# Kernel optimization log

Hardware: AMD Instinct MI355X
Metric: run time of the kernel (lower is better)

Reference implementation:

```python
import jax, jax.numpy as jnp
import numpy as np

M, N, D = 8192, 8192, 64

def setup_inputs() -> dict:
    key = jax.random.key(0)
    k1, k2 = jax.random.split(key)
    X = jax.random.normal(k1, (M, D), dtype=jnp.float32)
    Y = jax.random.normal(k2, (N, D), dtype=jnp.float32)
    gamma_param = jnp.asarray(1.0, dtype=jnp.float32)  # learnable scalar (rbf branch)
    return {"X": X, "Y": Y, "gamma_param": gamma_param}

def reference(X, Y, gamma_param):
    # RBF kernel: exp(-gamma * ||x_i - y_j||^2), (m, n)
    x_sq = jnp.sum(X * X, axis=-1)          # (m,)
    y_sq = jnp.sum(Y * Y, axis=-1)          # (n,)
    xy = jnp.einsum("md,nd->mn", X, Y)      # (m, n)
    sq_norm = x_sq[:, None] + y_sq[None, :] - 2.0 * xy
    sq_norm = jnp.maximum(sq_norm, 0.0)     # numerical clamp
    return jnp.exp(-gamma_param * sq_norm)
```

## Files before the change

kernel.cpp:

```cpp
#include <hip/hip_runtime.h>

#define MTOT 8192
#define NTOT 8192
#define DD   64
#define SPLIT (MTOT * DD)

typedef __bf16 bf16x8 __attribute__((ext_vector_type(8)));
typedef float  f32x16 __attribute__((ext_vector_type(16)));
typedef unsigned short u16;
typedef unsigned short u16x4 __attribute__((ext_vector_type(4)));
typedef unsigned short u16x8 __attribute__((ext_vector_type(8)));

__device__ __forceinline__ u16 bf16_rne(float v) {
    unsigned int u = __float_as_uint(v);
    u = u + 0x7FFFu + ((u >> 16) & 1u);
    return (u16)(u >> 16);
}
__device__ __forceinline__ float bf16_to_f32(u16 h) {
    return __uint_as_float(((unsigned int)h) << 16);
}

#define MFMA(a, b, c) __builtin_amdgcn_mfma_f32_32x32x16_bf16((a), (b), (c), 0, 0, 0)

__global__ __launch_bounds__(256)
void rbf_pre_kernel(const float* __restrict__ X, const float* __restrict__ Y,
                    u16* __restrict__ XhiF, u16* __restrict__ XloF,
                    u16* __restrict__ YhiF, u16* __restrict__ YloF,
                    float* __restrict__ xqs, float* __restrict__ yqs)
{
    const int gid = blockIdx.x * 256 + threadIdx.x;
    const int mat = gid >> 15;
    const int r4  = gid & 32767;
    const int row = r4 >> 2;
    const int q   = r4 & 3;
    const float* src = mat ? Y : X;
    u16* hi  = mat ? YhiF : XhiF;
    u16* lo  = mat ? YloF : XloF;
    float* nrm = mat ? yqs : xqs;

    const long rbase = (long)row * DD + q * 16;
    float s = 0.f;
    u16x8 h0, h1, l0, l1;
    #pragma unroll
    for (int c = 0; c < 4; ++c) {
        const float4 v = *reinterpret_cast<const float4*>(src + rbase + c * 4);
        const float vv[4] = {v.x, v.y, v.z, v.w};
        #pragma unroll
        for (int e = 0; e < 4; ++e) {
            const int idx = c * 4 + e;
            const float x = vv[e];
            s = fmaf(x, x, s);
            const u16 hh = bf16_rne(x);
            const u16 ll = bf16_rne(x - bf16_to_f32(hh));
            if (idx < 8) { h0[idx] = hh; l0[idx] = ll; }
            else         { h1[idx - 8] = hh; l1[idx - 8] = ll; }
        }
    }
    s += __shfl_xor(s, 1);
    s += __shfl_xor(s, 2);
    if (q == 0) nrm[row] = s;

    const int tt = row >> 5, lr = row & 31;
    const long fbase = (long)(tt * 4 + q) * 512;
    *reinterpret_cast<u16x8*>(hi + fbase + lr * 8)        = h0;
    *reinterpret_cast<u16x8*>(hi + fbase + (32 + lr) * 8) = h1;
    *reinterpret_cast<u16x8*>(lo + fbase + lr * 8)        = l0;
    *reinterpret_cast<u16x8*>(lo + fbase + (32 + lr) * 8) = l1;
}

__global__ __launch_bounds__(256, 2)
void rbf_main_kernel(const u16* __restrict__ XhiF, const u16* __restrict__ XloF,
                     const u16* __restrict__ YhiF, const u16* __restrict__ YloF,
                     const float* __restrict__ xqs, const float* __restrict__ yqs,
                     const float* __restrict__ gamma_p,
                     float* __restrict__ out)
{
    __shared__ __align__(16) u16 S[4][8192];

    const int t = threadIdx.x;
    const int w = t >> 6;
    const int l = t & 63;

    const int bid = blockIdx.x;
    const int swz = ((bid & 7) << 9) | (bid >> 3);
    const int bm = swz >> 6;
    const int bn = swz & 63;
    const long row0 = (long)bm * 128;
    const long col0 = (long)bn * 128;

    const u16* gsrc;
    if      (w == 0) gsrc = XhiF + (long)bm * 8192;
    else if (w == 1) gsrc = XloF + (long)bm * 8192;
    else if (w == 2) gsrc = YhiF + (long)bn * 8192;
    else             gsrc = YloF + (long)bn * 8192;
    u16* const ldst = &S[w][0];
    #pragma unroll
    for (int c = 0; c < 16; ++c) {
        const int off = c * 512 + l * 8;
        *reinterpret_cast<int4*>(ldst + off) = *reinterpret_cast<const int4*>(gsrc + off);
    }
    __syncthreads();

    const int mt0 = (w >> 1) * 2;
    const int nt0 = (w & 1) * 2;

    bf16x8 aH[2][4], aL[2][4];
    #pragma unroll
    for (int i = 0; i < 2; ++i)
        #pragma unroll
        for (int ks = 0; ks < 4; ++ks) {
            aH[i][ks] = *reinterpret_cast<const bf16x8*>(&S[0][((mt0 + i) * 4 + ks) * 512 + l * 8]);
            aL[i][ks] = *reinterpret_cast<const bf16x8*>(&S[1][((mt0 + i) * 4 + ks) * 512 + l * 8]);
        }

    f32x16 acc[2][2];
    #pragma unroll
    for (int i = 0; i < 2; ++i)
        #pragma unroll
        for (int j = 0; j < 2; ++j)
            #pragma unroll
            for (int r = 0; r < 16; ++r) acc[i][j][r] = 0.f;

    #pragma unroll
    for (int ks = 0; ks < 4; ++ks) {
        const bf16x8 b0h = *reinterpret_cast<const bf16x8*>(&S[2][((nt0 + 0) * 4 + ks) * 512 + l * 8]);
        const bf16x8 b1h = *reinterpret_cast<const bf16x8*>(&S[2][((nt0 + 1) * 4 + ks) * 512 + l * 8]);
        const bf16x8 b0l = *reinterpret_cast<const bf16x8*>(&S[3][((nt0 + 0) * 4 + ks) * 512 + l * 8]);
        const bf16x8 b1l = *reinterpret_cast<const bf16x8*>(&S[3][((nt0 + 1) * 4 + ks) * 512 + l * 8]);
        acc[0][0] = MFMA(aH[0][ks], b0h, acc[0][0]);
        acc[0][1] = MFMA(aH[0][ks], b1h, acc[0][1]);
        acc[1][0] = MFMA(aH[1][ks], b0h, acc[1][0]);
        acc[1][1] = MFMA(aH[1][ks], b1h, acc[1][1]);
        acc[0][0] = MFMA(aH[0][ks], b0l, acc[0][0]);
        acc[0][1] = MFMA(aH[0][ks], b1l, acc[0][1]);
        acc[1][0] = MFMA(aH[1][ks], b0l, acc[1][0]);
        acc[1][1] = MFMA(aH[1][ks], b1l, acc[1][1]);
        acc[0][0] = MFMA(aL[0][ks], b0h, acc[0][0]);
        acc[0][1] = MFMA(aL[0][ks], b1h, acc[0][1]);
        acc[1][0] = MFMA(aL[1][ks], b0h, acc[1][0]);
        acc[1][1] = MFMA(aL[1][ks], b1h, acc[1][1]);
    }

    const float g  = gamma_p[0];
    const float g2 = 2.0f * g;
    const int l5x4 = (l >> 5) * 4;
    const int ln   = l & 31;

    #pragma unroll
    for (int i = 0; i < 2; ++i) {
        const int mt = mt0 + i;
        float xv[16];
        #pragma unroll
        for (int p = 0; p < 4; ++p) {
            const float4 x4 = *reinterpret_cast<const float4*>(xqs + row0 + mt * 32 + 8 * p + l5x4);
            xv[p * 4 + 0] = x4.x; xv[p * 4 + 1] = x4.y;
            xv[p * 4 + 2] = x4.z; xv[p * 4 + 3] = x4.w;
        }
        #pragma unroll
        for (int j = 0; j < 2; ++j) {
            const int nt = nt0 + j;
            const long gc = col0 + nt * 32 + ln;
            const float cy = -g * yqs[gc];
            float* const obase = out + gc;
            #pragma unroll
            for (int r = 0; r < 16; ++r) {
                float arg = fmaf(g2, acc[i][j][r], fmaf(-g, xv[r], cy));
                arg = fminf(arg, 0.f);
                const long rr = row0 + mt * 32 + (r & 3) + 8 * (r >> 2) + l5x4;
                __builtin_nontemporal_store(__expf(arg), obase + rr * (long)NTOT);
            }
        }
    }
}

__global__ __launch_bounds__(256, 2)
void rbf_fallback_kernel(const float* __restrict__ X,
                         const float* __restrict__ Y,
                         const float* __restrict__ gamma_p,
                         float* __restrict__ out)
{
    __shared__ unsigned short XfH[4][4][64][8];
    __shared__ unsigned short XfL[4][4][64][8];
    __shared__ unsigned short YfH[4][4][64][8];
    __shared__ unsigned short YfL[4][4][64][8];
    __shared__ float xq[128];
    __shared__ float yq[128];

    const int t = threadIdx.x;
    const long row0 = (long)blockIdx.y * 128;
    const long col0 = (long)blockIdx.x * 128;

    {
        const int k0   = (t & 15) * 4;
        const int ks   = k0 >> 4;
        const int l32  = ((k0 >> 3) & 1) << 5;
        const int slot = k0 & 4;
        #pragma unroll
        for (int i = 0; i < 8; ++i) {
            const int row  = (t >> 4) + i * 16;
            const int mt   = row >> 5;
            const int lane = (row & 31) | l32;
            const float4 vx = *reinterpret_cast<const float4*>(X + (row0 + row) * DD + k0);
            const float4 vy = *reinterpret_cast<const float4*>(Y + (col0 + row) * DD + k0);
            float xv[4] = {vx.x, vx.y, vx.z, vx.w};
            float yv[4] = {vy.x, vy.y, vy.z, vy.w};
            u16x4 xh, xl, yh, yl;
            #pragma unroll
            for (int e = 0; e < 4; ++e) {
                const u16 hx = bf16_rne(xv[e]);
                xh[e] = hx; xl[e] = bf16_rne(xv[e] - bf16_to_f32(hx));
                const u16 hy = bf16_rne(yv[e]);
                yh[e] = hy; yl[e] = bf16_rne(yv[e] - bf16_to_f32(hy));
            }
            *reinterpret_cast<u16x4*>(&XfH[mt][ks][lane][slot]) = xh;
            *reinterpret_cast<u16x4*>(&XfL[mt][ks][lane][slot]) = xl;
            *reinterpret_cast<u16x4*>(&YfH[mt][ks][lane][slot]) = yh;
            *reinterpret_cast<u16x4*>(&YfL[mt][ks][lane][slot]) = yl;
        }
    }
    {
        const int r = t & 127;
        const float* p = (t < 128) ? (X + (row0 + r) * DD) : (Y + (col0 + r) * DD);
        float s0 = 0.f, s1 = 0.f, s2 = 0.f, s3 = 0.f;
        #pragma unroll
        for (int c = 0; c < 16; ++c) {
            const float4 v = reinterpret_cast<const float4*>(p)[c];
            s0 = fmaf(v.x, v.x, s0); s1 = fmaf(v.y, v.y, s1);
            s2 = fmaf(v.z, v.z, s2); s3 = fmaf(v.w, v.w, s3);
        }
        const float s = (s0 + s1) + (s2 + s3);
        if (t < 128) xq[r] = s; else yq[r] = s;
    }
    __syncthreads();

    const int w = t >> 6;
    const int l = t & 63;
    const int mt0 = (w >> 1) * 2;
    const int nt0 = (w & 1) * 2;

    bf16x8 aH[2][4], aL[2][4];
    #pragma unroll
    for (int i = 0; i < 2; ++i)
        #pragma unroll
        for (int ks = 0; ks < 4; ++ks) {
            aH[i][ks] = *reinterpret_cast<const bf16x8*>(&XfH[mt0 + i][ks][l][0]);
            aL[i][ks] = *reinterpret_cast<const bf16x8*>(&XfL[mt0 + i][ks][l][0]);
        }

    f32x16 acc[2][2];
    #pragma unroll
    for (int i = 0; i < 2; ++i)
        #pragma unroll
        for (int j = 0; j < 2; ++j)
            #pragma unroll
            for (int r = 0; r < 16; ++r) acc[i][j][r] = 0.f;

    #pragma unroll
    for (int ks = 0; ks < 4; ++ks) {
        const bf16x8 b0h = *reinterpret_cast<const bf16x8*>(&YfH[nt0 + 0][ks][l][0]);
        const bf16x8 b1h = *reinterpret_cast<const bf16x8*>(&YfH[nt0 + 1][ks][l][0]);
        const bf16x8 b0l = *reinterpret_cast<const bf16x8*>(&YfL[nt0 + 0][ks][l][0]);
        const bf16x8 b1l = *reinterpret_cast<const bf16x8*>(&YfL[nt0 + 1][ks][l][0]);
        acc[0][0] = MFMA(aH[0][ks], b0h, acc[0][0]);
        acc[0][1] = MFMA(aH[0][ks], b1h, acc[0][1]);
        acc[1][0] = MFMA(aH[1][ks], b0h, acc[1][0]);
        acc[1][1] = MFMA(aH[1][ks], b1h, acc[1][1]);
        acc[0][0] = MFMA(aH[0][ks], b0l, acc[0][0]);
        acc[0][1] = MFMA(aH[0][ks], b1l, acc[0][1]);
        acc[1][0] = MFMA(aH[1][ks], b0l, acc[1][0]);
        acc[1][1] = MFMA(aH[1][ks], b1l, acc[1][1]);
        acc[0][0] = MFMA(aL[0][ks], b0h, acc[0][0]);
        acc[0][1] = MFMA(aL[0][ks], b1h, acc[0][1]);
        acc[1][0] = MFMA(aL[1][ks], b0h, acc[1][0]);
        acc[1][1] = MFMA(aL[1][ks], b1h, acc[1][1]);
    }

    const float g = gamma_p[0];
    const int l5x4 = (l >> 5) * 4;
    const int ln = l & 31;
    #pragma unroll
    for (int i = 0; i < 2; ++i) {
        const int mt = mt0 + i;
        float xv[16];
        #pragma unroll
        for (int r = 0; r < 16; ++r)
            xv[r] = xq[mt * 32 + (r & 3) + 8 * (r >> 2) + l5x4];
        #pragma unroll
        for (int j = 0; j < 2; ++j) {
            const int nt = nt0 + j;
            const float yv = yq[nt * 32 + ln];
            const long gr = row0 + mt * 32;
            const long gc = col0 + nt * 32 + ln;
            #pragma unroll
            for (int r = 0; r < 16; ++r) {
                float s = fmaf(-2.f, acc[i][j][r], xv[r] + yv);
                s = fmaxf(s, 0.f);
                const long rr = gr + (r & 3) + 8 * (r >> 2) + l5x4;
                out[rr * NTOT + gc] = __expf(-g * s);
            }
        }
    }
}

extern "C" void kernel_launch(void* const* d_in, const int* in_sizes, int n_in,
                              void* d_out, int out_size, void* d_ws, size_t ws_size,
                              hipStream_t stream) {
    (void)in_sizes; (void)n_in; (void)out_size;
    const float* X = (const float*)d_in[0];
    const float* Y = (const float*)d_in[1];
    const float* gamma_p = (const float*)d_in[2];
    float* out = (float*)d_out;

    const size_t need = 4 * (size_t)SPLIT * sizeof(u16) + (MTOT + NTOT) * sizeof(float);

    if (ws_size >= need) {
        u16* XhiF = (u16*)d_ws;
        u16* XloF = XhiF + SPLIT;
        u16* YhiF = XloF + SPLIT;
        u16* YloF = YhiF + SPLIT;
        float* xqs = (float*)(YloF + SPLIT);
        float* yqs = xqs + MTOT;
        rbf_pre_kernel<<<256, 256, 0, stream>>>(X, Y, XhiF, XloF, YhiF, YloF, xqs, yqs);
        rbf_main_kernel<<<4096, 256, 0, stream>>>(XhiF, XloF, YhiF, YloF, xqs, yqs, gamma_p, out);
    } else {
        dim3 grid(NTOT / 128, MTOT / 128);
        rbf_fallback_kernel<<<grid, 256, 0, stream>>>(X, Y, gamma_p, out);
    }
}
```

Measured before the change: 56.13 us.

## Make RBF main kernel persistent, reusing X tiles and prefetching Y via LDS DMA

Replaces the one-tile-per-block main kernel with a 512-block persistent kernel. Each block keeps its X hi/lo tile resident and iterates over 8 column tiles. Y tiles are loaded with global_load_lds DMA, and the next one is issued before the exp/store epilogue so the load overlaps output writes. This removes repeated X loads and per-block launch and setup cost, but adds per-iteration barriers and less block-level parallelism for hiding store latency.

```diff
diff --git a/kernel.cpp b/kernel.cpp
--- a/kernel.cpp
+++ b/kernel.cpp
@@ -21,6 +21,13 @@
 }
 
 #define MFMA(a, b, c) __builtin_amdgcn_mfma_f32_32x32x16_bf16((a), (b), (c), 0, 0, 0)
+
+__device__ __forceinline__ void load_lds_16B(const u16* g, u16* lds_uniform) {
+    __builtin_amdgcn_global_load_lds(
+        (const __attribute__((address_space(1))) unsigned int*)g,
+        (__attribute__((address_space(3))) unsigned int*)lds_uniform,
+        16, 0, 0);
+}
 
 __global__ __launch_bounds__(256)
 void rbf_pre_kernel(const float* __restrict__ X, const float* __restrict__ Y,
@@ -69,107 +76,135 @@
 }
 
 __global__ __launch_bounds__(256, 2)
-void rbf_main_kernel(const u16* __restrict__ XhiF, const u16* __restrict__ XloF,
-                     const u16* __restrict__ YhiF, const u16* __restrict__ YloF,
-                     const float* __restrict__ xqs, const float* __restrict__ yqs,
-                     const float* __restrict__ gamma_p,
-                     float* __restrict__ out)
+void rbf_persist_kernel(const u16* __restrict__ XhiF, const u16* __restrict__ XloF,
+                        const u16* __restrict__ YhiF, const u16* __restrict__ YloF,
+                        const float* __restrict__ xqs, const float* __restrict__ yqs,
+                        const float* __restrict__ gamma_p,
+                        float* __restrict__ out)
 {
-    __shared__ __align__(16) u16 S[4][8192];
+    __shared__ __align__(16) u16 Xbuf[16384];
+    __shared__ __align__(16) u16 Ybuf[16384];
 
     const int t = threadIdx.x;
     const int w = t >> 6;
     const int l = t & 63;
 
-    const int bid = blockIdx.x;
-    const int swz = ((bid & 7) << 9) | (bid >> 3);
-    const int bm = swz >> 6;
-    const int bn = swz & 63;
+    const int p   = blockIdx.x;
+    const int xcd = p & 7;
+    const int i   = p >> 3;
+    const int bm  = xcd * 8 + (i >> 3);
+    const int bn0 = i & 7;
     const long row0 = (long)bm * 128;
-    const long col0 = (long)bn * 128;
-
-    const u16* gsrc;
-    if      (w == 0) gsrc = XhiF + (long)bm * 8192;
-    else if (w == 1) gsrc = XloF + (long)bm * 8192;
-    else if (w == 2) gsrc = YhiF + (long)bn * 8192;
-    else             gsrc = YloF + (long)bn * 8192;
-    u16* const ldst = &S[w][0];
-    #pragma unroll
-    for (int c = 0; c < 16; ++c) {
-        const int off = c * 512 + l * 8;
-        *reinterpret_cast<int4*>(ldst + off) = *reinterpret_cast<const int4*>(gsrc + off);
-    }
-    __syncthreads();
-
-    const int mt0 = (w >> 1) * 2;
-    const int nt0 = (w & 1) * 2;
-
-    bf16x8 aH[2][4], aL[2][4];
-    #pragma unroll
-    for (int i = 0; i < 2; ++i)
-        #pragma unroll
-        for (int ks = 0; ks < 4; ++ks) {
-            aH[i][ks] = *reinterpret_cast<const bf16x8*>(&S[0][((mt0 + i) * 4 + ks) * 512 + l * 8]);
-            aL[i][ks] = *reinterpret_cast<const bf16x8*>(&S[1][((mt0 + i) * 4 + ks) * 512 + l * 8]);
-        }
-
-    f32x16 acc[2][2];
-    #pragma unroll
-    for (int i = 0; i < 2; ++i)
-        #pragma unroll
-        for (int j = 0; j < 2; ++j)
-            #pragma unroll
-            for (int r = 0; r < 16; ++r) acc[i][j][r] = 0.f;
-
-    #pragma unroll
-    for (int ks = 0; ks < 4; ++ks) {
-        const bf16x8 b0h = *reinterpret_cast<const bf16x8*>(&S[2][((nt0 + 0) * 4 + ks) * 512 + l * 8]);
-        const bf16x8 b1h = *reinterpret_cast<const bf16x8*>(&S[2][((nt0 + 1) * 4 + ks) * 512 + l * 8]);
-        const bf16x8 b0l = *reinterpret_cast<const bf16x8*>(&S[3][((nt0 + 0) * 4 + ks) * 512 + l * 8]);
-        const bf16x8 b1l = *reinterpret_cast<const bf16x8*>(&S[3][((nt0 + 1) * 4 + ks) * 512 + l * 8]);
-        acc[0][0] = MFMA(aH[0][ks], b0h, acc[0][0]);
-        acc[0][1] = MFMA(aH[0][ks], b1h, acc[0][1]);
-        acc[1][0] = MFMA(aH[1][ks], b0h, acc[1][0]);
-        acc[1][1] = MFMA(aH[1][ks], b1h, acc[1][1]);
-        acc[0][0] = MFMA(aH[0][ks], b0l, acc[0][0]);
-        acc[0][1] = MFMA(aH[0][ks], b1l, acc[0][1]);
-        acc[1][0] = MFMA(aH[1][ks], b0l, acc[1][0]);
-        acc[1][1] = MFMA(aH[1][ks], b1l, acc[1][1]);
-        acc[0][0] = MFMA(aL[0][ks], b0h, acc[0][0]);
-        acc[0][1] = MFMA(aL[0][ks], b1h, acc[0][1]);
-        acc[1][0] = MFMA(aL[1][ks], b0h, acc[1][0]);
-        acc[1][1] = MFMA(aL[1][ks], b1h, acc[1][1]);
+
+    {
+        const u16* xh = XhiF + (long)bm * 8192;
+        const u16* xl = XloF + (long)bm * 8192;
+        const u16* yh = YhiF + (long)bn0 * 8192;
+        const u16* yl = YloF + (long)bn0 * 8192;
+        #pragma unroll
+        for (int cc = 0; cc < 8; ++cc) {
+            const int c = w * 8 + cc;
+            const u16* gx = (c < 16) ? (xh + c * 512) : (xl + (c - 16) * 512);
+            const u16* gy = (c < 16) ? (yh + c * 512) : (yl + (c - 16) * 512);
+            load_lds_16B(gx + l * 8, &Xbuf[c * 512]);
+            load_lds_16B(gy + l * 8, &Ybuf[c * 512]);
+        }
     }
 
     const float g  = gamma_p[0];
     const float g2 = 2.0f * g;
+    const int  mt0 = (w >> 1) * 2;
+    const int  nt0 = (w & 1) * 2;
     const int l5x4 = (l >> 5) * 4;
-    const int ln   = l & 31;
-
-    #pragma unroll
-    for (int i = 0; i < 2; ++i) {
-        const int mt = mt0 + i;
-        float xv[16];
-        #pragma unroll
-        for (int p = 0; p < 4; ++p) {
-            const float4 x4 = *reinterpret_cast<const float4*>(xqs + row0 + mt * 32 + 8 * p + l5x4);
-            xv[p * 4 + 0] = x4.x; xv[p * 4 + 1] = x4.y;
-            xv[p * 4 + 2] = x4.z; xv[p * 4 + 3] = x4.w;
-        }
-        #pragma unroll
-        for (int j = 0; j < 2; ++j) {
-            const int nt = nt0 + j;
-            const long gc = col0 + nt * 32 + ln;
-            const float cy = -g * yqs[gc];
-            float* const obase = out + gc;
-            #pragma unroll
-            for (int r = 0; r < 16; ++r) {
-                float arg = fmaf(g2, acc[i][j][r], fmaf(-g, xv[r], cy));
-                arg = fminf(arg, 0.f);
-                const long rr = row0 + mt * 32 + (r & 3) + 8 * (r >> 2) + l5x4;
-                __builtin_nontemporal_store(__expf(arg), obase + rr * (long)NTOT);
+    const int  ln  = l & 31;
+
+    float xv[2][16];
+    #pragma unroll
+    for (int ii = 0; ii < 2; ++ii)
+        #pragma unroll
+        for (int q4 = 0; q4 < 4; ++q4) {
+            const float4 x4 = *reinterpret_cast<const float4*>(
+                xqs + row0 + (mt0 + ii) * 32 + 8 * q4 + l5x4);
+            xv[ii][q4 * 4 + 0] = x4.x; xv[ii][q4 * 4 + 1] = x4.y;
+            xv[ii][q4 * 4 + 2] = x4.z; xv[ii][q4 * 4 + 3] = x4.w;
+        }
+
+    __syncthreads();
+
+    bf16x8 aH[2][4], aL[2][4];
+    #pragma unroll
+    for (int ii = 0; ii < 2; ++ii)
+        #pragma unroll
+        for (int ks = 0; ks < 4; ++ks) {
+            aH[ii][ks] = *reinterpret_cast<const bf16x8*>(&Xbuf[((mt0 + ii) * 4 + ks) * 512 + l * 8]);
+            aL[ii][ks] = *reinterpret_cast<const bf16x8*>(&Xbuf[8192 + ((mt0 + ii) * 4 + ks) * 512 + l * 8]);
+        }
+
+    for (int it = 0; it < 8; ++it) {
+        const int  bn   = bn0 + 8 * it;
+        const long col0 = (long)bn * 128;
+
+        f32x16 acc[2][2];
+        #pragma unroll
+        for (int ii = 0; ii < 2; ++ii)
+            #pragma unroll
+            for (int jj = 0; jj < 2; ++jj)
+                #pragma unroll
+                for (int r = 0; r < 16; ++r) acc[ii][jj][r] = 0.f;
+
+        #pragma unroll
+        for (int ks = 0; ks < 4; ++ks) {
+            const bf16x8 b0h = *reinterpret_cast<const bf16x8*>(&Ybuf[((nt0 + 0) * 4 + ks) * 512 + l * 8]);
+            const bf16x8 b1h = *reinterpret_cast<const bf16x8*>(&Ybuf[((nt0 + 1) * 4 + ks) * 512 + l * 8]);
+            const bf16x8 b0l = *reinterpret_cast<const bf16x8*>(&Ybuf[8192 + ((nt0 + 0) * 4 + ks) * 512 + l * 8]);
+            const bf16x8 b1l = *reinterpret_cast<const bf16x8*>(&Ybuf[8192 + ((nt0 + 1) * 4 + ks) * 512 + l * 8]);
+            acc[0][0] = MFMA(aH[0][ks], b0h, acc[0][0]);
+            acc[0][1] = MFMA(aH[0][ks], b1h, acc[0][1]);
+            acc[1][0] = MFMA(aH[1][ks], b0h, acc[1][0]);
+            acc[1][1] = MFMA(aH[1][ks], b1h, acc[1][1]);
+            acc[0][0] = MFMA(aH[0][ks], b0l, acc[0][0]);
+            acc[0][1] = MFMA(aH[0][ks], b1l, acc[0][1]);
+            acc[1][0] = MFMA(aH[1][ks], b0l, acc[1][0]);
+            acc[1][1] = MFMA(aH[1][ks], b1l, acc[1][1]);
+            acc[0][0] = MFMA(aL[0][ks], b0h, acc[0][0]);
+            acc[0][1] = MFMA(aL[0][ks], b1h, acc[0][1]);
+            acc[1][0] = MFMA(aL[1][ks], b0h, acc[1][0]);
+            acc[1][1] = MFMA(aL[1][ks], b1h, acc[1][1]);
+        }
+
+        __syncthreads();
+
+        if (it < 7) {
+            const int bnn = bn0 + 8 * (it + 1);
+            const u16* yh = YhiF + (long)bnn * 8192;
+            const u16* yl = YloF + (long)bnn * 8192;
+            #pragma unroll
+            for (int cc = 0; cc < 8; ++cc) {
+                const int c = w * 8 + cc;
+                const u16* gy = (c < 16) ? (yh + c * 512) : (yl + (c - 16) * 512);
+                load_lds_16B(gy + l * 8, &Ybuf[c * 512]);
             }
         }
+
+        #pragma unroll
+        for (int ii = 0; ii < 2; ++ii) {
+            const int mt = mt0 + ii;
+            float* const orow = out + (row0 + mt * 32) * (long)NTOT;
+            #pragma unroll
+            for (int jj = 0; jj < 2; ++jj) {
+                const long gc = col0 + (nt0 + jj) * 32 + ln;
+                const float cy = -g * yqs[gc];
+                #pragma unroll
+                for (int r = 0; r < 16; ++r) {
+                    float arg = fmaf(g2, acc[ii][jj][r], fmaf(-g, xv[ii][r], cy));
+                    arg = fminf(arg, 0.f);
+                    const int rr = (r & 3) + 8 * (r >> 2) + l5x4;
+                    __builtin_nontemporal_store(__expf(arg), orow + rr * (long)NTOT + gc);
+                }
+            }
+        }
+
+        if (it < 7) __syncthreads();
     }
 }
 
@@ -220,11 +255,11 @@
     }
     {
         const int r = t & 127;
-        const float* p = (t < 128) ? (X + (row0 + r) * DD) : (Y + (col0 + r) * DD);
+        const float* p2 = (t < 128) ? (X + (row0 + r) * DD) : (Y + (col0 + r) * DD);
         float s0 = 0.f, s1 = 0.f, s2 = 0.f, s3 = 0.f;
         #pragma unroll
         for (int c = 0; c < 16; ++c) {
-            const float4 v = reinterpret_cast<const float4*>(p)[c];
+            const float4 v = reinterpret_cast<const float4*>(p2)[c];
             s0 = fmaf(v.x, v.x, s0); s1 = fmaf(v.y, v.y, s1);
             s2 = fmaf(v.z, v.z, s2); s3 = fmaf(v.w, v.w, s3);
         }
@@ -321,7 +356,7 @@
         float* xqs = (float*)(YloF + SPLIT);
         float* yqs = xqs + MTOT;
         rbf_pre_kernel<<<256, 256, 0, stream>>>(X, Y, XhiF, XloF, YhiF, YloF, xqs, yqs);
-        rbf_main_kernel<<<4096, 256, 0, stream>>>(XhiF, XloF, YhiF, YloF, xqs, yqs, gamma_p, out);
+        rbf_persist_kernel<<<512, 256, 0, stream>>>(XhiF, XloF, YhiF, YloF, xqs, yqs, gamma_p, out);
     } else {
         dim3 grid(NTOT / 128, MTOT / 128);
         rbf_fallback_kernel<<<grid, 256, 0, stream>>>(X, Y, gamma_p, out);
```

Result: slower. 61.84 us (+10.2%).

## Load MFMA fragments directly from global memory, dropping LDS staging

Applied to the files above, without the earlier changes.

The main kernel no longer stages the pre-swizzled bf16 hi/lo fragments through 64 KB of shared memory. Each wave now reads its A and B fragments straight from global memory, with a one-step register prefetch across the k-loop, and the occupancy hint rises from 2 to 3 blocks per CU. This removes the LDS round trip and the block barrier, and the freed shared memory can allow more resident blocks to hide the store-bound epilogue. In exchange, each fragment is read twice from global/L2 (once by each of two waves) instead of once per block.

```diff
diff --git a/kernel.cpp b/kernel.cpp
--- a/kernel.cpp
+++ b/kernel.cpp
@@ -68,18 +68,17 @@
     *reinterpret_cast<u16x8*>(lo + fbase + (32 + lr) * 8) = l1;
 }
 
-__global__ __launch_bounds__(256, 2)
-void rbf_main_kernel(const u16* __restrict__ XhiF, const u16* __restrict__ XloF,
-                     const u16* __restrict__ YhiF, const u16* __restrict__ YloF,
-                     const float* __restrict__ xqs, const float* __restrict__ yqs,
-                     const float* __restrict__ gamma_p,
-                     float* __restrict__ out)
+__global__ __launch_bounds__(256, 3)
+void rbf_nolds_kernel(const u16* __restrict__ XhiF, const u16* __restrict__ XloF,
+                      const u16* __restrict__ YhiF, const u16* __restrict__ YloF,
+                      const float* __restrict__ xqs, const float* __restrict__ yqs,
+                      const float* __restrict__ gamma_p,
+                      float* __restrict__ out)
 {
-    __shared__ __align__(16) u16 S[4][8192];
-
     const int t = threadIdx.x;
     const int w = t >> 6;
     const int l = t & 63;
+    const int loff = l * 8;
 
     const int bid = blockIdx.x;
     const int swz = ((bid & 7) << 9) | (bid >> 3);
@@ -88,86 +87,84 @@
     const long row0 = (long)bm * 128;
     const long col0 = (long)bn * 128;
 
-    const u16* gsrc;
-    if      (w == 0) gsrc = XhiF + (long)bm * 8192;
-    else if (w == 1) gsrc = XloF + (long)bm * 8192;
-    else if (w == 2) gsrc = YhiF + (long)bn * 8192;
-    else             gsrc = YloF + (long)bn * 8192;
-    u16* const ldst = &S[w][0];
-    #pragma unroll
-    for (int c = 0; c < 16; ++c) {
-        const int off = c * 512 + l * 8;
-        *reinterpret_cast<int4*>(ldst + off) = *reinterpret_cast<const int4*>(gsrc + off);
-    }
-    __syncthreads();
-
     const int mt0 = (w >> 1) * 2;
     const int nt0 = (w & 1) * 2;
 
-    bf16x8 aH[2][4], aL[2][4];
-    #pragma unroll
-    for (int i = 0; i < 2; ++i)
-        #pragma unroll
-        for (int ks = 0; ks < 4; ++ks) {
-            aH[i][ks] = *reinterpret_cast<const bf16x8*>(&S[0][((mt0 + i) * 4 + ks) * 512 + l * 8]);
-            aL[i][ks] = *reinterpret_cast<const bf16x8*>(&S[1][((mt0 + i) * 4 + ks) * 512 + l * 8]);
-        }
+    const u16* const xh = XhiF + (long)bm * 8192;
+    const u16* const xl = XloF + (long)bm * 8192;
+    const u16* const yh = YhiF + (long)bn * 8192;
+    const u16* const yl = YloF + (long)bn * 8192;
+
+#define FRAG(base, tt, ks) (*reinterpret_cast<const bf16x8*>((base) + ((tt) * 4 + (ks)) * 512 + loff))
 
     f32x16 acc[2][2];
     #pragma unroll
-    for (int i = 0; i < 2; ++i)
-        #pragma unroll
-        for (int j = 0; j < 2; ++j)
-            #pragma unroll
-            for (int r = 0; r < 16; ++r) acc[i][j][r] = 0.f;
+    for (int ii = 0; ii < 2; ++ii)
+        #pragma unroll
+        for (int jj = 0; jj < 2; ++jj)
+            #pragma unroll
+            for (int r = 0; r < 16; ++r) acc[ii][jj][r] = 0.f;
+
+    bf16x8 cAH0 = FRAG(xh, mt0 + 0, 0), cAH1 = FRAG(xh, mt0 + 1, 0);
+    bf16x8 cAL0 = FRAG(xl, mt0 + 0, 0), cAL1 = FRAG(xl, mt0 + 1, 0);
+    bf16x8 cBH0 = FRAG(yh, nt0 + 0, 0), cBH1 = FRAG(yh, nt0 + 1, 0);
+    bf16x8 cBL0 = FRAG(yl, nt0 + 0, 0), cBL1 = FRAG(yl, nt0 + 1, 0);
 
     #pragma unroll
     for (int ks = 0; ks < 4; ++ks) {
-        const bf16x8 b0h = *reinterpret_cast<const bf16x8*>(&S[2][((nt0 + 0) * 4 + ks) * 512 + l * 8]);
-        const bf16x8 b1h = *reinterpret_cast<const bf16x8*>(&S[2][((nt0 + 1) * 4 + ks) * 512 + l * 8]);
-        const bf16x8 b0l = *reinterpret_cast<const bf16x8*>(&S[3][((nt0 + 0) * 4 + ks) * 512 + l * 8]);
-        const bf16x8 b1l = *reinterpret_cast<const bf16x8*>(&S[3][((nt0 + 1) * 4 + ks) * 512 + l * 8]);
-        acc[0][0] = MFMA(aH[0][ks], b0h, acc[0][0]);
-        acc[0][1] = MFMA(aH[0][ks], b1h, acc[0][1]);
-        acc[1][0] = MFMA(aH[1][ks], b0h, acc[1][0]);
-        acc[1][1] = MFMA(aH[1][ks], b1h, acc[1][1]);
-        acc[0][0] = MFMA(aH[0][ks], b0l, acc[0][0]);
-        acc[0][1] = MFMA(aH[0][ks], b1l, acc[0][1]);
-        acc[1][0] = MFMA(aH[1][ks], b0l, acc[1][0]);
-        acc[1][1] = MFMA(aH[1][ks], b1l, acc[1][1]);
-        acc[0][0] = MFMA(aL[0][ks], b0h, acc[0][0]);
-        acc[0][1] = MFMA(aL[0][ks], b1h, acc[0][1]);
-        acc[1][0] = MFMA(aL[1][ks], b0h, acc[1][0]);
-        acc[1][1] = MFMA(aL[1][ks], b1h, acc[1][1]);
-    }
+        bf16x8 nAH0, nAH1, nAL0, nAL1, nBH0, nBH1, nBL0, nBL1;
+        if (ks < 3) {
+            nAH0 = FRAG(xh, mt0 + 0, ks + 1); nAH1 = FRAG(xh, mt0 + 1, ks + 1);
+            nAL0 = FRAG(xl, mt0 + 0, ks + 1); nAL1 = FRAG(xl, mt0 + 1, ks + 1);
+            nBH0 = FRAG(yh, nt0 + 0, ks + 1); nBH1 = FRAG(yh, nt0 + 1, ks + 1);
+            nBL0 = FRAG(yl, nt0 + 0, ks + 1); nBL1 = FRAG(yl, nt0 + 1, ks + 1);
+        }
+        acc[0][0] = MFMA(cAH0, cBH0, acc[0][0]);
+        acc[0][1] = MFMA(cAH0, cBH1, acc[0][1]);
+        acc[1][0] = MFMA(cAH1, cBH0, acc[1][0]);
+        acc[1][1] = MFMA(cAH1, cBH1, acc[1][1]);
+        acc[0][0] = MFMA(cAH0, cBL0, acc[0][0]);
+        acc[0][1] = MFMA(cAH0, cBL1, acc[0][1]);
+        acc[1][0] = MFMA(cAH1, cBL0, acc[1][0]);
+        acc[1][1] = MFMA(cAH1, cBL1, acc[1][1]);
+        acc[0][0] = MFMA(cAL0, cBH0, acc[0][0]);
+        acc[0][1] = MFMA(cAL0, cBH1, acc[0][1]);
+        acc[1][0] = MFMA(cAL1, cBH0, acc[1][0]);
+        acc[1][1] = MFMA(cAL1, cBH1, acc[1][1]);
+        if (ks < 3) {
+            cAH0 = nAH0; cAH1 = nAH1; cAL0 = nAL0; cAL1 = nAL1;
+            cBH0 = nBH0; cBH1 = nBH1; cBL0 = nBL0; cBL1 = nBL1;
+        }
+    }
+#undef FRAG
 
     const float g  = gamma_p[0];
     const float g2 = 2.0f * g;
     const int l5x4 = (l >> 5) * 4;
-    const int ln   = l & 31;
-
-    #pragma unroll
-    for (int i = 0; i < 2; ++i) {
-        const int mt = mt0 + i;
+    const int  ln  = l & 31;
+
+    #pragma unroll
+    for (int ii = 0; ii < 2; ++ii) {
+        const int mt = mt0 + ii;
         float xv[16];
         #pragma unroll
-        for (int p = 0; p < 4; ++p) {
-            const float4 x4 = *reinterpret_cast<const float4*>(xqs + row0 + mt * 32 + 8 * p + l5x4);
-            xv[p * 4 + 0] = x4.x; xv[p * 4 + 1] = x4.y;
-            xv[p * 4 + 2] = x4.z; xv[p * 4 + 3] = x4.w;
-        }
-        #pragma unroll
-        for (int j = 0; j < 2; ++j) {
-            const int nt = nt0 + j;
-            const long gc = col0 + nt * 32 + ln;
+        for (int q4 = 0; q4 < 4; ++q4) {
+            const float4 x4 = *reinterpret_cast<const float4*>(
+                xqs + row0 + mt * 32 + 8 * q4 + l5x4);
+            xv[q4 * 4 + 0] = x4.x; xv[q4 * 4 + 1] = x4.y;
+            xv[q4 * 4 + 2] = x4.z; xv[q4 * 4 + 3] = x4.w;
+        }
+        float* const orow = out + (row0 + mt * 32) * (long)NTOT;
+        #pragma unroll
+        for (int jj = 0; jj < 2; ++jj) {
+            const long gc = col0 + (nt0 + jj) * 32 + ln;
             const float cy = -g * yqs[gc];
-            float* const obase = out + gc;
             #pragma unroll
             for (int r = 0; r < 16; ++r) {
-                float arg = fmaf(g2, acc[i][j][r], fmaf(-g, xv[r], cy));
+                float arg = fmaf(g2, acc[ii][jj][r], fmaf(-g, xv[r], cy));
                 arg = fminf(arg, 0.f);
-                const long rr = row0 + mt * 32 + (r & 3) + 8 * (r >> 2) + l5x4;
-                __builtin_nontemporal_store(__expf(arg), obase + rr * (long)NTOT);
+                const int rr = (r & 3) + 8 * (r >> 2) + l5x4;
+                __builtin_nontemporal_store(__expf(arg), orow + rr * (long)NTOT + gc);
             }
         }
     }
@@ -220,11 +217,11 @@
     }
     {
         const int r = t & 127;
-        const float* p = (t < 128) ? (X + (row0 + r) * DD) : (Y + (col0 + r) * DD);
+        const float* p2 = (t < 128) ? (X + (row0 + r) * DD) : (Y + (col0 + r) * DD);
         float s0 = 0.f, s1 = 0.f, s2 = 0.f, s3 = 0.f;
         #pragma unroll
         for (int c = 0; c < 16; ++c) {
-            const float4 v = reinterpret_cast<const float4*>(p)[c];
+            const float4 v = reinterpret_cast<const float4*>(p2)[c];
             s0 = fmaf(v.x, v.x, s0); s1 = fmaf(v.y, v.y, s1);
             s2 = fmaf(v.z, v.z, s2); s3 = fmaf(v.w, v.w, s3);
         }
@@ -321,7 +318,7 @@
         float* xqs = (float*)(YloF + SPLIT);
         float* yqs = xqs + MTOT;
         rbf_pre_kernel<<<256, 256, 0, stream>>>(X, Y, XhiF, XloF, YhiF, YloF, xqs, yqs);
-        rbf_main_kernel<<<4096, 256, 0, stream>>>(XhiF, XloF, YhiF, YloF, xqs, yqs, gamma_p, out);
+        rbf_nolds_kernel<<<4096, 256, 0, stream>>>(XhiF, XloF, YhiF, YloF, xqs, yqs, gamma_p, out);
     } else {
         dim3 grid(NTOT / 128, MTOT / 128);
         rbf_fallback_kernel<<<grid, 256, 0, stream>>>(X, Y, gamma_p, out);
```

After: 68.69 us. 1.22x slower.

## Load tiles via direct global-to-LDS, prefetch norms, and compute one output subtile at a time

Applied to the files above, without the earlier changes.

The main kernel now copies the bf16 hi/lo tiles straight from global memory into LDS with global_load_lds, so the data no longer passes through VGPRs. It also loads the x and y norm values before the barrier so their latency overlaps the tile load. The MFMA work is reordered to compute and store one 32x32 accumulator at a time instead of holding all four, which lowers register pressure and lets the exp and store epilogue interleave with the next MFMAs. The cost is reloading the B fragments from LDS for each subtile.

```diff
diff --git a/kernel.cpp b/kernel.cpp
--- a/kernel.cpp
+++ b/kernel.cpp
@@ -21,6 +21,13 @@
 }
 
 #define MFMA(a, b, c) __builtin_amdgcn_mfma_f32_32x32x16_bf16((a), (b), (c), 0, 0, 0)
+
+__device__ __forceinline__ void load_lds_16B(const u16* g, u16* lds_uniform) {
+    __builtin_amdgcn_global_load_lds(
+        (const __attribute__((address_space(1))) unsigned int*)g,
+        (__attribute__((address_space(3))) unsigned int*)lds_uniform,
+        16, 0, 0);
+}
 
 __global__ __launch_bounds__(256)
 void rbf_pre_kernel(const float* __restrict__ X, const float* __restrict__ Y,
@@ -69,17 +76,18 @@
 }
 
 __global__ __launch_bounds__(256, 2)
-void rbf_main_kernel(const u16* __restrict__ XhiF, const u16* __restrict__ XloF,
-                     const u16* __restrict__ YhiF, const u16* __restrict__ YloF,
-                     const float* __restrict__ xqs, const float* __restrict__ yqs,
-                     const float* __restrict__ gamma_p,
-                     float* __restrict__ out)
+void rbf_fused_kernel(const u16* __restrict__ XhiF, const u16* __restrict__ XloF,
+                      const u16* __restrict__ YhiF, const u16* __restrict__ YloF,
+                      const float* __restrict__ xqs, const float* __restrict__ yqs,
+                      const float* __restrict__ gamma_p,
+                      float* __restrict__ out)
 {
     __shared__ __align__(16) u16 S[4][8192];
 
     const int t = threadIdx.x;
     const int w = t >> 6;
     const int l = t & 63;
+    const int loff = l * 8;
 
     const int bid = blockIdx.x;
     const int swz = ((bid & 7) << 9) | (bid >> 3);
@@ -88,87 +96,82 @@
     const long row0 = (long)bm * 128;
     const long col0 = (long)bn * 128;
 
-    const u16* gsrc;
-    if      (w == 0) gsrc = XhiF + (long)bm * 8192;
-    else if (w == 1) gsrc = XloF + (long)bm * 8192;
-    else if (w == 2) gsrc = YhiF + (long)bn * 8192;
-    else             gsrc = YloF + (long)bn * 8192;
-    u16* const ldst = &S[w][0];
-    #pragma unroll
-    for (int c = 0; c < 16; ++c) {
-        const int off = c * 512 + l * 8;
-        *reinterpret_cast<int4*>(ldst + off) = *reinterpret_cast<const int4*>(gsrc + off);
-    }
-    __syncthreads();
-
-    const int mt0 = (w >> 1) * 2;
-    const int nt0 = (w & 1) * 2;
-
-    bf16x8 aH[2][4], aL[2][4];
-    #pragma unroll
-    for (int i = 0; i < 2; ++i)
-        #pragma unroll
-        for (int ks = 0; ks < 4; ++ks) {
-            aH[i][ks] = *reinterpret_cast<const bf16x8*>(&S[0][((mt0 + i) * 4 + ks) * 512 + l * 8]);
-            aL[i][ks] = *reinterpret_cast<const bf16x8*>(&S[1][((mt0 + i) * 4 + ks) * 512 + l * 8]);
-        }
-
-    f32x16 acc[2][2];
-    #pragma unroll
-    for (int i = 0; i < 2; ++i)
-        #pragma unroll
-        for (int j = 0; j < 2; ++j)
-            #pragma unroll
-            for (int r = 0; r < 16; ++r) acc[i][j][r] = 0.f;
-
-    #pragma unroll
-    for (int ks = 0; ks < 4; ++ks) {
-        const bf16x8 b0h = *reinterpret_cast<const bf16x8*>(&S[2][((nt0 + 0) * 4 + ks) * 512 + l * 8]);
-        const bf16x8 b1h = *reinterpret_cast<const bf16x8*>(&S[2][((nt0 + 1) * 4 + ks) * 512 + l * 8]);
-        const bf16x8 b0l = *reinterpret_cast<const bf16x8*>(&S[3][((nt0 + 0) * 4 + ks) * 512 + l * 8]);
-        const bf16x8 b1l = *reinterpret_cast<const bf16x8*>(&S[3][((nt0 + 1) * 4 + ks) * 512 + l * 8]);
-        acc[0][0] = MFMA(aH[0][ks], b0h, acc[0][0]);
-        acc[0][1] = MFMA(aH[0][ks], b1h, acc[0][1]);
-        acc[1][0] = MFMA(aH[1][ks], b0h, acc[1][0]);
-        acc[1][1] = MFMA(aH[1][ks], b1h, acc[1][1]);
-        acc[0][0] = MFMA(aH[0][ks], b0l, acc[0][0]);
-        acc[0][1] = MFMA(aH[0][ks], b1l, acc[0][1]);
-        acc[1][0] = MFMA(aH[1][ks], b0l, acc[1][0]);
-        acc[1][1] = MFMA(aH[1][ks], b1l, acc[1][1]);
-        acc[0][0] = MFMA(aL[0][ks], b0h, acc[0][0]);
-        acc[0][1] = MFMA(aL[0][ks], b1h, acc[0][1]);
-        acc[1][0] = MFMA(aL[1][ks], b0h, acc[1][0]);
-        acc[1][1] = MFMA(aL[1][ks], b1h, acc[1][1]);
+    {
+        const u16* gsrc;
+        if      (w == 0) gsrc = XhiF + (long)bm * 8192;
+        else if (w == 1) gsrc = XloF + (long)bm * 8192;
+        else if (w == 2) gsrc = YhiF + (long)bn * 8192;
+        else             gsrc = YloF + (long)bn * 8192;
+        #pragma unroll
+        for (int c = 0; c < 16; ++c)
+            load_lds_16B(gsrc + c * 512 + loff, &S[w][c * 512]);
     }
 
     const float g  = gamma_p[0];
     const float g2 = 2.0f * g;
+    const int  mt0 = (w >> 1) * 2;
+    const int  nt0 = (w & 1) * 2;
     const int l5x4 = (l >> 5) * 4;
-    const int ln   = l & 31;
-
-    #pragma unroll
-    for (int i = 0; i < 2; ++i) {
-        const int mt = mt0 + i;
-        float xv[16];
-        #pragma unroll
-        for (int p = 0; p < 4; ++p) {
-            const float4 x4 = *reinterpret_cast<const float4*>(xqs + row0 + mt * 32 + 8 * p + l5x4);
-            xv[p * 4 + 0] = x4.x; xv[p * 4 + 1] = x4.y;
-            xv[p * 4 + 2] = x4.z; xv[p * 4 + 3] = x4.w;
-        }
-        #pragma unroll
-        for (int j = 0; j < 2; ++j) {
-            const int nt = nt0 + j;
-            const long gc = col0 + nt * 32 + ln;
-            const float cy = -g * yqs[gc];
-            float* const obase = out + gc;
-            #pragma unroll
-            for (int r = 0; r < 16; ++r) {
-                float arg = fmaf(g2, acc[i][j][r], fmaf(-g, xv[r], cy));
-                arg = fminf(arg, 0.f);
-                const long rr = row0 + mt * 32 + (r & 3) + 8 * (r >> 2) + l5x4;
-                __builtin_nontemporal_store(__expf(arg), obase + rr * (long)NTOT);
-            }
+    const int  ln  = l & 31;
+
+    float xv[2][16];
+    #pragma unroll
+    for (int ii = 0; ii < 2; ++ii)
+        #pragma unroll
+        for (int q4 = 0; q4 < 4; ++q4) {
+            const float4 x4 = *reinterpret_cast<const float4*>(
+                xqs + row0 + (mt0 + ii) * 32 + 8 * q4 + l5x4);
+            xv[ii][q4 * 4 + 0] = x4.x; xv[ii][q4 * 4 + 1] = x4.y;
+            xv[ii][q4 * 4 + 2] = x4.z; xv[ii][q4 * 4 + 3] = x4.w;
+        }
+    float cy[2];
+    #pragma unroll
+    for (int jj = 0; jj < 2; ++jj)
+        cy[jj] = -g * yqs[col0 + (nt0 + jj) * 32 + ln];
+
+    __syncthreads();
+
+    bf16x8 aH[2][4], aL[2][4];
+    #pragma unroll
+    for (int ii = 0; ii < 2; ++ii)
+        #pragma unroll
+        for (int ks = 0; ks < 4; ++ks) {
+            aH[ii][ks] = *reinterpret_cast<const bf16x8*>(&S[0][((mt0 + ii) * 4 + ks) * 512 + loff]);
+            aL[ii][ks] = *reinterpret_cast<const bf16x8*>(&S[1][((mt0 + ii) * 4 + ks) * 512 + loff]);
+        }
+
+    #pragma unroll
+    for (int qq = 0; qq < 4; ++qq) {
+        const int ii = qq & 1;
+        const int jj = qq >> 1;
+
+        bf16x8 bH[4], bL[4];
+        #pragma unroll
+        for (int ks = 0; ks < 4; ++ks) {
+            bH[ks] = *reinterpret_cast<const bf16x8*>(&S[2][((nt0 + jj) * 4 + ks) * 512 + loff]);
+            bL[ks] = *reinterpret_cast<const bf16x8*>(&S[3][((nt0 + jj) * 4 + ks) * 512 + loff]);
+        }
+
+        f32x16 acc;
+        #pragma unroll
+        for (int r = 0; r < 16; ++r) acc[r] = 0.f;
+        #pragma unroll
+        for (int ks = 0; ks < 4; ++ks) {
+            acc = MFMA(aH[ii][ks], bH[ks], acc);
+            acc = MFMA(aH[ii][ks], bL[ks], acc);
+            acc = MFMA(aL[ii][ks], bH[ks], acc);
+        }
+
+        const int  mt  = mt0 + ii;
+        const long gc  = col0 + (nt0 + jj) * 32 + ln;
+        float* const orow = out + (row0 + mt * 32) * (long)NTOT + gc;
+        const float cyj = cy[jj];
+        #pragma unroll
+        for (int r = 0; r < 16; ++r) {
+            float arg = fmaf(g2, acc[r], fmaf(-g, xv[ii][r], cyj));
+            arg = fminf(arg, 0.f);
+            const int rr = (r & 3) + 8 * (r >> 2) + l5x4;
+            __builtin_nontemporal_store(__expf(arg), orow + rr * (long)NTOT);
         }
     }
 }
@@ -220,11 +223,11 @@
     }
     {
         const int r = t & 127;
-        const float* p = (t < 128) ? (X + (row0 + r) * DD) : (Y + (col0 + r) * DD);
+        const float* p2 = (t < 128) ? (X + (row0 + r) * DD) : (Y + (col0 + r) * DD);
         float s0 = 0.f, s1 = 0.f, s2 = 0.f, s3 = 0.f;
         #pragma unroll
         for (int c = 0; c < 16; ++c) {
-            const float4 v = reinterpret_cast<const float4*>(p)[c];
+            const float4 v = reinterpret_cast<const float4*>(p2)[c];
             s0 = fmaf(v.x, v.x, s0); s1 = fmaf(v.y, v.y, s1);
             s2 = fmaf(v.z, v.z, s2); s3 = fmaf(v.w, v.w, s3);
         }
@@ -321,7 +324,7 @@
         float* xqs = (float*)(YloF + SPLIT);
         float* yqs = xqs + MTOT;
         rbf_pre_kernel<<<256, 256, 0, stream>>>(X, Y, XhiF, XloF, YhiF, YloF, xqs, yqs);
-        rbf_main_kernel<<<4096, 256, 0, stream>>>(XhiF, XloF, YhiF, YloF, xqs, yqs, gamma_p, out);
+        rbf_fused_kernel<<<4096, 256, 0, stream>>>(XhiF, XloF, YhiF, YloF, xqs, yqs, gamma_p, out);
     } else {
         dim3 grid(NTOT / 128, MTOT / 128);
         rbf_fallback_kernel<<<grid, 256, 0, stream>>>(X, Y, gamma_p, out);
```

Result: slower. 57.44 us (+2.3%).
